# Kernel tuning notes

Hardware: AMD Instinct MI355X
Metric: run time of the kernel (lower is better)

## Reference

```python
import jax, jax.numpy as jnp
import numpy as np

NUM_CLASSES = 6
CE_W, DICE_W, FT_W = 0.4, 0.4, 0.2
FT_ALPHA, FT_BETA, FT_GAMMA = 0.7, 0.3, 1.33


def setup_inputs() -> dict:
    key = jax.random.key(0)
    k1, k2 = jax.random.split(key)
    logits = jax.random.normal(k1, (16, NUM_CLASSES, 512, 512), dtype=jnp.float32)
    targets = jax.random.randint(k2, (16, 512, 512), 0, NUM_CLASSES, dtype=jnp.int64)
    return {"logits": logits, "targets": targets}


def reference(logits, targets):
    B, C, H, W = logits.shape
    # ---- shared: log-softmax / softmax over class dim (computed once) ----
    logp = jax.nn.log_softmax(logits, axis=1)          # (B,C,H,W)
    probs = jnp.exp(logp)

    # ---- Cross entropy (mean over all pixels) ----
    lp_t = jnp.take_along_axis(logp, targets[:, None, :, :], axis=1)[:, 0]  # (B,H,W)
    ce = -lp_t.mean()

    # ---- per-class sufficient statistics (no full one-hot kept around) ----
    oh = (targets[:, None, :, :] == jnp.arange(C, dtype=targets.dtype)[None, :, None, None])
    oh = oh.astype(probs.dtype)                         # (B,C,H,W)
    TP = jnp.sum(probs * oh, axis=(2, 3))               # (B,C)
    p_sum = jnp.sum(probs, axis=(2, 3))                 # (B,C)
    t_sum = jnp.sum(oh, axis=(2, 3))                    # (B,C)

    # ---- Dice ----
    dice = (2.0 * TP + 1e-8) / (p_sum + t_sum + 1e-8)   # (B,C)
    dice_loss = jnp.mean(1.0 - dice)                    # mean over B and C

    # ---- Focal Tversky ----
    FP = p_sum - TP
    FN = t_sum - TP
    tversky = (TP + 1e-6) / (TP + FT_ALPHA * FN + FT_BETA * FP + 1e-6)
    ft_loss = jnp.mean((1.0 - tversky) ** FT_GAMMA)

    return CE_W * ce + DICE_W * dice_loss + FT_W * ft_loss
```

## Files before the change

### kernel.cpp

```cpp
#include <hip/hip_runtime.h>

#define BATCH 16
#define NCLS 6
#define HW 262144
#define BLOCKS_PER_B 64
#define THREADS 256
#define ITERS 4

#define NACC 19

__global__ __launch_bounds__(THREADS) void loss_main(
    const float* __restrict__ logits,
    const int*   __restrict__ targets,
    float*       __restrict__ ws) {
    const int b   = blockIdx.y;
    const int bx  = blockIdx.x;
    const int tid = threadIdx.x;

    float facc[13];
    #pragma unroll
    for (int i = 0; i < 13; ++i) facc[i] = 0.f;
    int tcnt[NCLS];
    #pragma unroll
    for (int c = 0; c < NCLS; ++c) tcnt[c] = 0;

    const float* lbase = logits + (size_t)b * NCLS * HW;
    const int4*  tbase = (const int4*)(targets + (size_t)b * HW);

    for (int k = 0; k < ITERS; ++k) {
        const int p4 = k * (BLOCKS_PER_B * THREADS) + bx * THREADS + tid;

        float L[4][NCLS];
        #pragma unroll
        for (int c = 0; c < NCLS; ++c) {
            float4 v = ((const float4*)(lbase + (size_t)c * HW))[p4];
            L[0][c] = v.x; L[1][c] = v.y; L[2][c] = v.z; L[3][c] = v.w;
        }
        const int4 tv4 = tbase[p4];
        const int tgt[4] = {tv4.x, tv4.y, tv4.z, tv4.w};

        #pragma unroll
        for (int j = 0; j < 4; ++j) {
            float m = L[j][0];
            #pragma unroll
            for (int c = 1; c < NCLS; ++c) m = fmaxf(m, L[j][c]);

            float e[NCLS];
            float s = 0.f;
            #pragma unroll
            for (int c = 0; c < NCLS; ++c) { e[c] = __expf(L[j][c] - m); s += e[c]; }
            const float inv = __builtin_amdgcn_rcpf(s);
            const float lse = m + __logf(s);

            float Lt = 0.f;
            #pragma unroll
            for (int c = 0; c < NCLS; ++c) {
                const float pr = e[c] * inv;
                facc[6 + c] += pr;
                const bool is_t = (tgt[j] == c);
                facc[c] += is_t ? pr : 0.f;
                Lt = is_t ? L[j][c] : Lt;
                tcnt[c] += (int)__popcll(__ballot(is_t));
            }
            facc[12] += lse - Lt;
        }
    }

    #pragma unroll
    for (int i = 0; i < 13; ++i) {
        float v = facc[i];
        v += __shfl_down(v, 32);
        v += __shfl_down(v, 16);
        v += __shfl_down(v, 8);
        v += __shfl_down(v, 4);
        v += __shfl_down(v, 2);
        v += __shfl_down(v, 1);
        facc[i] = v;
    }

    __shared__ float sacc[NACC];
    if (tid < NACC) sacc[tid] = 0.f;
    __syncthreads();
    if ((tid & 63) == 0) {
        #pragma unroll
        for (int i = 0; i < 6; ++i) atomicAdd(&sacc[i], facc[i]);
        #pragma unroll
        for (int i = 0; i < 6; ++i) atomicAdd(&sacc[6 + i], facc[6 + i]);
        #pragma unroll
        for (int c = 0; c < NCLS; ++c) atomicAdd(&sacc[12 + c], (float)tcnt[c]);
        atomicAdd(&sacc[18], facc[12]);
    }
    __syncthreads();
    if (tid < NACC)
        ws[(tid * BATCH + b) * BLOCKS_PER_B + bx] = sacc[tid];
}

__global__ __launch_bounds__(128) void loss_finalize(
    const float* __restrict__ ws, float* __restrict__ out) {
    __shared__ float sd[128], sf[128], sc[128];
    const int i = threadIdx.x;
    float dice = 0.f, ft = 0.f, ce = 0.f;
    if (i < BATCH * NCLS) {
        const int b = i / NCLS, c = i % NCLS;
        float TP = 0.f, PS = 0.f, TS = 0.f;
        #pragma unroll 8
        for (int k = 0; k < BLOCKS_PER_B; ++k) {
            TP += ws[((c)      * BATCH + b) * BLOCKS_PER_B + k];
            PS += ws[((6 + c)  * BATCH + b) * BLOCKS_PER_B + k];
            TS += ws[((12 + c) * BATCH + b) * BLOCKS_PER_B + k];
        }
        const float d = (2.f * TP + 1e-8f) / (PS + TS + 1e-8f);
        dice = 1.f - d;
        const float FP = PS - TP;
        const float FN = TS - TP;
        const float tv = (TP + 1e-6f) / (TP + 0.7f * FN + 0.3f * FP + 1e-6f);
        ft = powf(fmaxf(1.f - tv, 0.f), 1.33f);
    }
    if (i < BATCH) {
        #pragma unroll 8
        for (int k = 0; k < BLOCKS_PER_B; ++k)
            ce += ws[(18 * BATCH + i) * BLOCKS_PER_B + k];
    }
    sd[i] = dice; sf[i] = ft; sc[i] = ce;
    __syncthreads();
    for (int s = 64; s > 0; s >>= 1) {
        if (i < s) { sd[i] += sd[i + s]; sf[i] += sf[i + s]; sc[i] += sc[i + s]; }
        __syncthreads();
    }
    if (i == 0) {
        const float ce_mean   = sc[0] / (float)((size_t)BATCH * HW);
        const float dice_loss = sd[0] / (float)(BATCH * NCLS);
        const float ft_loss   = sf[0] / (float)(BATCH * NCLS);
        out[0] = 0.4f * ce_mean + 0.4f * dice_loss + 0.2f * ft_loss;
    }
}

extern "C" void kernel_launch(void* const* d_in, const int* in_sizes, int n_in,
                              void* d_out, int out_size, void* d_ws, size_t ws_size,
                              hipStream_t stream) {
    const float* logits  = (const float*)d_in[0];
    const int*   targets = (const int*)d_in[1];
    float*       ws      = (float*)d_ws;

    loss_main<<<dim3(BLOCKS_PER_B, BATCH), THREADS, 0, stream>>>(logits, targets, ws);
    loss_finalize<<<1, 128, 0, stream>>>(ws, (float*)d_out);
}
```

Measured before the change: 168.0 us.

## Issue all loads up front, double block count, and coalesce workspace reduction

The main kernel doubles the blocks per batch and halves per-thread iterations. Each thread now issues all of its logit and target loads before any compute, putting more memory requests in flight to hide latency. The workspace layout becomes block-major so the finalize kernel can sum 304 rows with coalesced reads across 320 threads instead of strided per-row loops. The cost is higher register pressure from holding all loaded data at once and more partial sums to reduce.

```diff
diff --git a/kernel.cpp b/kernel.cpp
--- a/kernel.cpp
+++ b/kernel.cpp
@@ -3,11 +3,12 @@
 #define BATCH 16
 #define NCLS 6
 #define HW 262144
-#define BLOCKS_PER_B 64
+#define BLOCKS_PER_B 128
 #define THREADS 256
-#define ITERS 4
+#define KITER 2
 
 #define NACC 19
+#define NROW (NACC * BATCH)
 
 __global__ __launch_bounds__(THREADS) void loss_main(
     const float* __restrict__ logits,
@@ -17,6 +18,20 @@
     const int bx  = blockIdx.x;
     const int tid = threadIdx.x;
 
+    const float* lbase = logits + (size_t)b * NCLS * HW;
+    const int4*  tbase = (const int4*)(targets + (size_t)b * HW);
+
+    float4 va[KITER][NCLS];
+    int4   tv[KITER];
+    #pragma unroll
+    for (int k = 0; k < KITER; ++k) {
+        const int p4 = k * (BLOCKS_PER_B * THREADS) + bx * THREADS + tid;
+        #pragma unroll
+        for (int c = 0; c < NCLS; ++c)
+            va[k][c] = ((const float4*)(lbase + (size_t)c * HW))[p4];
+        tv[k] = tbase[p4];
+    }
+
     float facc[13];
     #pragma unroll
     for (int i = 0; i < 13; ++i) facc[i] = 0.f;
@@ -24,31 +39,25 @@
     #pragma unroll
     for (int c = 0; c < NCLS; ++c) tcnt[c] = 0;
 
-    const float* lbase = logits + (size_t)b * NCLS * HW;
-    const int4*  tbase = (const int4*)(targets + (size_t)b * HW);
-
-    for (int k = 0; k < ITERS; ++k) {
-        const int p4 = k * (BLOCKS_PER_B * THREADS) + bx * THREADS + tid;
-
-        float L[4][NCLS];
-        #pragma unroll
-        for (int c = 0; c < NCLS; ++c) {
-            float4 v = ((const float4*)(lbase + (size_t)c * HW))[p4];
-            L[0][c] = v.x; L[1][c] = v.y; L[2][c] = v.z; L[3][c] = v.w;
-        }
-        const int4 tv4 = tbase[p4];
-        const int tgt[4] = {tv4.x, tv4.y, tv4.z, tv4.w};
-
+    #pragma unroll
+    for (int k = 0; k < KITER; ++k) {
+        const int tgt[4] = {tv[k].x, tv[k].y, tv[k].z, tv[k].w};
         #pragma unroll
         for (int j = 0; j < 4; ++j) {
-            float m = L[j][0];
+            float L[NCLS];
             #pragma unroll
-            for (int c = 1; c < NCLS; ++c) m = fmaxf(m, L[j][c]);
+            for (int c = 0; c < NCLS; ++c)
+                L[c] = (j == 0) ? va[k][c].x : (j == 1) ? va[k][c].y
+                     : (j == 2) ? va[k][c].z : va[k][c].w;
+
+            float m = L[0];
+            #pragma unroll
+            for (int c = 1; c < NCLS; ++c) m = fmaxf(m, L[c]);
 
             float e[NCLS];
             float s = 0.f;
             #pragma unroll
-            for (int c = 0; c < NCLS; ++c) { e[c] = __expf(L[j][c] - m); s += e[c]; }
+            for (int c = 0; c < NCLS; ++c) { e[c] = __expf(L[c] - m); s += e[c]; }
             const float inv = __builtin_amdgcn_rcpf(s);
             const float lse = m + __logf(s);
 
@@ -59,7 +68,7 @@
                 facc[6 + c] += pr;
                 const bool is_t = (tgt[j] == c);
                 facc[c] += is_t ? pr : 0.f;
-                Lt = is_t ? L[j][c] : Lt;
+                Lt = is_t ? L[c] : Lt;
                 tcnt[c] += (int)__popcll(__ballot(is_t));
             }
             facc[12] += lse - Lt;
@@ -83,51 +92,56 @@
     __syncthreads();
     if ((tid & 63) == 0) {
         #pragma unroll
-        for (int i = 0; i < 6; ++i) atomicAdd(&sacc[i], facc[i]);
+        for (int i = 0; i < 6; ++i)  atomicAdd(&sacc[i], facc[i]);
         #pragma unroll
-        for (int i = 0; i < 6; ++i) atomicAdd(&sacc[6 + i], facc[6 + i]);
+        for (int i = 0; i < 6; ++i)  atomicAdd(&sacc[6 + i], facc[6 + i]);
         #pragma unroll
         for (int c = 0; c < NCLS; ++c) atomicAdd(&sacc[12 + c], (float)tcnt[c]);
         atomicAdd(&sacc[18], facc[12]);
     }
     __syncthreads();
     if (tid < NACC)
-        ws[(tid * BATCH + b) * BLOCKS_PER_B + bx] = sacc[tid];
+        ws[bx * NROW + tid * BATCH + b] = sacc[tid];
 }
 
-__global__ __launch_bounds__(128) void loss_finalize(
+__global__ __launch_bounds__(320) void loss_finalize(
     const float* __restrict__ ws, float* __restrict__ out) {
+    __shared__ float rowsum[NROW];
     __shared__ float sd[128], sf[128], sc[128];
-    const int i = threadIdx.x;
-    float dice = 0.f, ft = 0.f, ce = 0.f;
-    if (i < BATCH * NCLS) {
-        const int b = i / NCLS, c = i % NCLS;
-        float TP = 0.f, PS = 0.f, TS = 0.f;
-        #pragma unroll 8
-        for (int k = 0; k < BLOCKS_PER_B; ++k) {
-            TP += ws[((c)      * BATCH + b) * BLOCKS_PER_B + k];
-            PS += ws[((6 + c)  * BATCH + b) * BLOCKS_PER_B + k];
-            TS += ws[((12 + c) * BATCH + b) * BLOCKS_PER_B + k];
+    const int t = threadIdx.x;
+
+    if (t < NROW) {
+        float s = 0.f;
+        #pragma unroll 16
+        for (int k = 0; k < BLOCKS_PER_B; ++k)
+            s += ws[k * NROW + t];
+        rowsum[t] = s;
+    }
+    __syncthreads();
+
+    if (t < 128) {
+        float dice = 0.f, ft = 0.f, ce = 0.f;
+        if (t < BATCH * NCLS) {
+            const int b = t / NCLS, c = t % NCLS;
+            const float TP = rowsum[c * BATCH + b];
+            const float PS = rowsum[(6 + c) * BATCH + b];
+            const float TS = rowsum[(12 + c) * BATCH + b];
+            const float d = (2.f * TP + 1e-8f) / (PS + TS + 1e-8f);
+            dice = 1.f - d;
+            const float FP = PS - TP;
+            const float FN = TS - TP;
+            const float tvk = (TP + 1e-6f) / (TP + 0.7f * FN + 0.3f * FP + 1e-6f);
+            ft = powf(fmaxf(1.f - tvk, 0.f), 1.33f);
         }
-        const float d = (2.f * TP + 1e-8f) / (PS + TS + 1e-8f);
-        dice = 1.f - d;
-        const float FP = PS - TP;
-        const float FN = TS - TP;
-        const float tv = (TP + 1e-6f) / (TP + 0.7f * FN + 0.3f * FP + 1e-6f);
-        ft = powf(fmaxf(1.f - tv, 0.f), 1.33f);
+        if (t < BATCH) ce = rowsum[18 * BATCH + t];
+        sd[t] = dice; sf[t] = ft; sc[t] = ce;
     }
-    if (i < BATCH) {
-        #pragma unroll 8
-        for (int k = 0; k < BLOCKS_PER_B; ++k)
-            ce += ws[(18 * BATCH + i) * BLOCKS_PER_B + k];
-    }
-    sd[i] = dice; sf[i] = ft; sc[i] = ce;
     __syncthreads();
     for (int s = 64; s > 0; s >>= 1) {
-        if (i < s) { sd[i] += sd[i + s]; sf[i] += sf[i + s]; sc[i] += sc[i + s]; }
+        if (t < s) { sd[t] += sd[t + s]; sf[t] += sf[t + s]; sc[t] += sc[t + s]; }
         __syncthreads();
     }
-    if (i == 0) {
+    if (t == 0) {
         const float ce_mean   = sc[0] / (float)((size_t)BATCH * HW);
         const float dice_loss = sd[0] / (float)(BATCH * NCLS);
         const float ft_loss   = sf[0] / (float)(BATCH * NCLS);
@@ -143,5 +157,5 @@
     float*       ws      = (float*)d_ws;
 
     loss_main<<<dim3(BLOCKS_PER_B, BATCH), THREADS, 0, stream>>>(logits, targets, ws);
-    loss_finalize<<<1, 128, 0, stream>>>(ws, (float*)d_out);
+    loss_finalize<<<1, 320, 0, stream>>>(ws, (float*)d_out);
 }
```

Result: no change. 165.7 us (-1.4%).
